# Kernel optimization log

Measured on AMD Instinct MI355X. Metric: run time of the kernel, lower is better.

Reference implementation:

```python
import jax, jax.numpy as jnp
import numpy as np

B, S, D, F, T, NS, L, H = 8, 1024, 1024, 4096, 64, 512, 32, 16
TAG_RATE = 0.5      # config.tagging_rate
GSR = 0.5           # config.gate_scaling_rate
ATT_EPS = 1e-12     # config.layer_norm_eps (att_norm)
ENC_EPS = 1e-5      # torch TransformerEncoderLayer default


def _ln(x, g, b, eps):
    m = x.mean(-1, keepdims=True)
    v = x.var(-1, keepdims=True)
    return (x - m) * jax.lax.rsqrt(v + eps) * g + b


def _rope(x):
    # standard rotary embedding over the full hidden dim
    d = x.shape[-1]
    s = x.shape[1]
    inv = 1.0 / (10000.0 ** (jnp.arange(0, d, 2, dtype=jnp.float32) / d))
    ang = jnp.arange(s, dtype=jnp.float32)[:, None] * inv[None, :]  # [S, D/2]
    sin, cos = jnp.sin(ang), jnp.cos(ang)
    x1, x2 = x[..., 0::2], x[..., 1::2]
    return jnp.stack([x1 * cos - x2 * sin, x1 * sin + x2 * cos], axis=-1).reshape(x.shape)


def setup_inputs() -> dict:
    key = jax.random.key(0)
    ks = jax.random.split(key, 24)
    p = lambda k, shp: (0.02 * jax.random.normal(k, shp, dtype=jnp.float32))
    inp = {
        'word_embedding': jax.random.normal(ks[0], (B, S, D), dtype=jnp.float32),
        'attention_mask': jnp.ones((B, S), dtype=jnp.int32),
        'span_batch': jax.random.randint(ks[1], (NS,), 0, B, dtype=jnp.int32),
        'span_start': jax.random.randint(ks[2], (NS,), 0, S - L, dtype=jnp.int32),
        'span_tag': jax.random.randint(ks[3], (NS,), 0, T, dtype=jnp.int32),
        'tag_emb': p(ks[4], (T, D)),
        'gate_w': p(ks[5], (D, 1)),
        'gate_b': jnp.zeros((1,), jnp.float32),
        'attn_ln_g': jnp.ones((D,), jnp.float32),
        'attn_ln_b': jnp.zeros((D,), jnp.float32),
        'in_proj_w': p(ks[6], (3 * D, D)),
        'in_proj_b': jnp.zeros((3 * D,), jnp.float32),
        'out_proj_w': p(ks[7], (D, D)),
        'out_proj_b': jnp.zeros((D,), jnp.float32),
        'enc_ln1_g': jnp.ones((D,), jnp.float32),
        'enc_ln1_b': jnp.zeros((D,), jnp.float32),
        'lin1_w': p(ks[8], (F, D)),
        'lin1_b': jnp.zeros((F,), jnp.float32),
        'lin2_w': p(ks[9], (D, F)),
        'lin2_b': jnp.zeros((D,), jnp.float32),
        'enc_ln2_g': jnp.ones((D,), jnp.float32),
        'enc_ln2_b': jnp.zeros((D,), jnp.float32),
    }
    return inp


def _mha(x, pad, in_proj_w, in_proj_b, out_proj_w, out_proj_b):
    b, s, d = x.shape
    hd = d // H
    qkv = x @ in_proj_w.T + in_proj_b                       # [B,S,3D]
    q, k, v = jnp.split(qkv, 3, axis=-1)
    rs = lambda t: t.reshape(b, s, H, hd).transpose(0, 2, 1, 3)  # [B,H,S,hd]
    q, k, v = rs(q), rs(k), rs(v)
    scores = jnp.einsum('bhqd,bhkd->bhqk', q, k) / jnp.sqrt(jnp.float32(hd))
    scores = jnp.where(pad[:, None, None, :], jnp.float32(-1e30), scores)
    attn = jax.nn.softmax(scores, axis=-1)
    o = jnp.einsum('bhqk,bhkd->bhqd', attn, v).transpose(0, 2, 1, 3).reshape(b, s, d)
    return o @ out_proj_w.T + out_proj_b


def reference(word_embedding, attention_mask, span_batch, span_start, span_tag,
              tag_emb, gate_w, gate_b, attn_ln_g, attn_ln_b,
              in_proj_w, in_proj_b, out_proj_w, out_proj_b,
              enc_ln1_g, enc_ln1_b, lin1_w, lin1_b, lin2_w, lin2_b,
              enc_ln2_g, enc_ln2_b):
    raw = word_embedding                        # dropout off (eval)
    we = _rope(word_embedding)
    # ragged gather -> gate -> scatter-add over fixed-length spans
    tok = span_start[:, None] + jnp.arange(L, dtype=jnp.int32)[None, :]  # [NS,L]
    X = we[span_batch[:, None], tok]            # [NS,L,D]
    gate = GSR * jax.nn.sigmoid(X @ gate_w + gate_b) + (1.0 - GSR) / 2.0  # [NS,L,1]
    res = gate * tag_emb[span_tag][:, None, :] * jnp.float32(L)          # [NS,L,D]
    taged = jnp.zeros_like(word_embedding).at[span_batch[:, None], tok].add(res)
    out_emb = raw + taged * TAG_RATE            # if_merge_by_add
    out_emb = _ln(out_emb, attn_ln_g, attn_ln_b, ATT_EPS)
    pad = attention_mask == 0
    # torch TransformerEncoderLayer (post-norm, relu)
    a = _mha(out_emb, pad, in_proj_w, in_proj_b, out_proj_w, out_proj_b)
    x = _ln(out_emb + a, enc_ln1_g, enc_ln1_b, ENC_EPS)
    ff = jax.nn.relu(x @ lin1_w.T + lin1_b) @ lin2_w.T + lin2_b
    enc = _ln(x + ff, enc_ln2_g, enc_ln2_b, ENC_EPS)
    return enc + out_emb
```

## Files before the change

### kernel.cpp

```cpp
#include <hip/hip_runtime.h>

#define DEV __device__ __forceinline__

typedef short bf16x8 __attribute__((ext_vector_type(8)));
typedef float f32x4 __attribute__((ext_vector_type(4)));
typedef unsigned short u16;
typedef unsigned int u32;

typedef __attribute__((address_space(3))) void lds_void;
typedef __attribute__((address_space(1))) void gbl_void;

DEV void async_copy16(void* lds_dst, const void* g_src) {
    __builtin_amdgcn_global_load_lds((gbl_void*)g_src, (lds_void*)lds_dst, 16, 0, 0);
}

DEV u16 f2bf(float x) {
    u32 u = __float_as_uint(x);
    return (u16)((u + 0x7fffu + ((u >> 16) & 1u)) >> 16);
}
DEV u16 f2bf_fast(float x) {
    return (u16)((__float_as_uint(x) + 0x8000u) >> 16);
}
DEV float bf2f(u16 v) { return __uint_as_float(((u32)v) << 16); }

__global__ __launch_bounds__(256) void f2bf_kernel(const float* __restrict__ src,
                                                   u16* __restrict__ dst, int n4) {
    const int i = blockIdx.x * 256 + threadIdx.x;
    if (i < n4) {
        const float4 v = ((const float4*)src)[i];
        ushort4 o;
        o.x = f2bf(v.x); o.y = f2bf(v.y); o.z = f2bf(v.z); o.w = f2bf(v.w);
        ((ushort4*)dst)[i] = o;
    }
}

__global__ __launch_bounds__(256) void span_kernel(
    const float* __restrict__ we, const int* __restrict__ sb,
    const int* __restrict__ ss, const int* __restrict__ stg,
    const float* __restrict__ tag_emb, const float* __restrict__ gate_w,
    const float* __restrict__ gate_b, float* __restrict__ out_pre) {
    __shared__ float red[4];
    const int n = blockIdx.x >> 5;
    const int l = blockIdx.x & 31;
    const int t = threadIdx.x;
    const int b = sb[n];
    const int s = ss[n] + l;
    const int tag = stg[n];
    const long base = ((long)b * 1024 + s) * 1024;
    float dot = 0.f;
#pragma unroll
    for (int pp = 0; pp < 2; ++pp) {
        const int p = t + pp * 256;
        const float e1 = we[base + 2 * p];
        const float e2 = we[base + 2 * p + 1];
        const float inv = exp2f((float)p * (-13.287712379549449f / 512.0f));
        const float ang = (float)s * inv;
        const float sa = __sinf(ang), ca = __cosf(ang);
        const float r1 = e1 * ca - e2 * sa;
        const float r2 = e1 * sa + e2 * ca;
        dot += r1 * gate_w[2 * p] + r2 * gate_w[2 * p + 1];
    }
#pragma unroll
    for (int off = 32; off > 0; off >>= 1) dot += __shfl_xor(dot, off, 64);
    if ((t & 63) == 0) red[t >> 6] = dot;
    __syncthreads();
    const float z = red[0] + red[1] + red[2] + red[3] + gate_b[0];
    const float gate = 0.25f + 0.5f / (1.f + __expf(-z));
    const float coef = gate * 16.f;
    const float* te = tag_emb + (long)tag * 1024;
#pragma unroll
    for (int c = 0; c < 4; ++c) {
        const int d = t + c * 256;
        atomicAdd(&out_pre[base + d], coef * te[d]);
    }
}

template <bool WRITE_F32, bool WRITE_BF, bool FINAL>
__global__ __launch_bounds__(256) void ln_kernel(
    const float* __restrict__ X, const float* __restrict__ g,
    const float* __restrict__ bta, float eps, float* __restrict__ Yf,
    u16* __restrict__ Ybf, const u16* __restrict__ addend) {
    __shared__ float red[8];
    const long row = blockIdx.x;
    const int t = threadIdx.x;
    const float4 x = ((const float4*)(X + row * 1024))[t];
    float s = x.x + x.y + x.z + x.w;
#pragma unroll
    for (int off = 32; off > 0; off >>= 1) s += __shfl_xor(s, off, 64);
    if ((t & 63) == 0) red[t >> 6] = s;
    __syncthreads();
    const float mean = (red[0] + red[1] + red[2] + red[3]) * (1.f / 1024.f);
    float4 dx;
    dx.x = x.x - mean; dx.y = x.y - mean; dx.z = x.z - mean; dx.w = x.w - mean;
    float ss = dx.x * dx.x + dx.y * dx.y + dx.z * dx.z + dx.w * dx.w;
#pragma unroll
    for (int off = 32; off > 0; off >>= 1) ss += __shfl_xor(ss, off, 64);
    if ((t & 63) == 0) red[4 + (t >> 6)] = ss;
    __syncthreads();
    const float var = (red[4] + red[5] + red[6] + red[7]) * (1.f / 1024.f);
    const float rstd = rsqrtf(var + eps);
    const float4 gv = ((const float4*)g)[t];
    const float4 bv = ((const float4*)bta)[t];
    float4 y;
    y.x = dx.x * rstd * gv.x + bv.x;
    y.y = dx.y * rstd * gv.y + bv.y;
    y.z = dx.z * rstd * gv.z + bv.z;
    y.w = dx.w * rstd * gv.w + bv.w;
    if (FINAL) {
        const ushort4 a = ((const ushort4*)(addend + row * 1024))[t];
        y.x += bf2f(a.x); y.y += bf2f(a.y); y.z += bf2f(a.z); y.w += bf2f(a.w);
    }
    if (WRITE_F32) ((float4*)(Yf + row * 1024))[t] = y;
    if (WRITE_BF) {
        ushort4 o;
        o.x = f2bf(y.x); o.y = f2bf(y.y); o.z = f2bf(y.z); o.w = f2bf(y.w);
        ((ushort4*)(Ybf + row * 1024))[t] = o;
    }
}

template <bool OUT_BF16, bool RELU, bool HAS_RES>
__global__ __launch_bounds__(256, 2) void gemm_nt(
    const u16* __restrict__ A, const u16* __restrict__ B,
    const float* __restrict__ bias, const u16* __restrict__ res,
    void* __restrict__ Cout, int N, int K) {
    __shared__ u16 Al[8192];
    __shared__ u16 Bl[8192];
    const int tid = threadIdx.x;
    const int wave = tid >> 6;
    const int lane = tid & 63;
    const int quad = lane >> 4;
    const int lq = lane & 15;
    const int wm = wave >> 1;
    const int wn = wave & 1;
    const long rowBase = (long)blockIdx.x * 128;
    const long colBase = (long)blockIdx.y * 128;

    f32x4 acc[4][4];
    const f32x4 fzero = {0.f, 0.f, 0.f, 0.f};
#pragma unroll
    for (int i = 0; i < 4; ++i)
#pragma unroll
        for (int j = 0; j < 4; ++j) acc[i][j] = fzero;

    const int rX = tid >> 3;
    const int pX = (tid & 7) ^ (rX & 7);
    const u16* gA = A + (rowBase + rX) * (long)K + pX * 8;
    const u16* gB = B + (colBase + rX) * (long)K + pX * 8;
    u16* ldsA = Al + wave * 512;
    u16* ldsB = Bl + wave * 512;

    for (int kt = 0; kt < K; kt += 64) {
        __syncthreads();
#pragma unroll
        for (int c = 0; c < 4; ++c) {
            async_copy16(ldsA + c * 2048, gA + (long)c * 32 * K + kt);
            async_copy16(ldsB + c * 2048, gB + (long)c * 32 * K + kt);
        }
        __syncthreads();
#pragma unroll
        for (int ks = 0; ks < 2; ++ks) {
            bf16x8 af[4], bfr[4];
#pragma unroll
            for (int i = 0; i < 4; ++i) {
                const int r = wm * 64 + i * 16 + lq;
                af[i] = *(const bf16x8*)&Al[r * 64 + (((ks * 4 + quad) ^ (lq & 7)) * 8)];
            }
#pragma unroll
            for (int j = 0; j < 4; ++j) {
                const int r = wn * 64 + j * 16 + lq;
                bfr[j] = *(const bf16x8*)&Bl[r * 64 + (((ks * 4 + quad) ^ (lq & 7)) * 8)];
            }
#pragma unroll
            for (int i = 0; i < 4; ++i)
#pragma unroll
                for (int j = 0; j < 4; ++j)
                    acc[i][j] = __builtin_amdgcn_mfma_f32_16x16x32_bf16(
                        af[i], bfr[j], acc[i][j], 0, 0, 0);
        }
    }

    float biasv[4];
#pragma unroll
    for (int j = 0; j < 4; ++j) biasv[j] = bias[colBase + wn * 64 + j * 16 + lq];
#pragma unroll
    for (int i = 0; i < 4; ++i) {
        const long grow = rowBase + wm * 64 + i * 16 + quad * 4;
#pragma unroll
        for (int j = 0; j < 4; ++j) {
            const long gcol = colBase + wn * 64 + j * 16 + lq;
#pragma unroll
            for (int r = 0; r < 4; ++r) {
                float v = acc[i][j][r] + biasv[j];
                if (RELU) v = fmaxf(v, 0.f);
                if (HAS_RES) v += bf2f(res[(grow + r) * N + gcol]);
                if (OUT_BF16)
                    ((u16*)Cout)[(grow + r) * N + gcol] = f2bf(v);
                else
                    ((float*)Cout)[(grow + r) * N + gcol] = v;
            }
        }
    }
}

template <bool OUT_BF16, bool RELU, bool HAS_RES>
__global__ __launch_bounds__(256, 4) void gemm_nt_m64(
    const u16* __restrict__ A, const u16* __restrict__ B,
    const float* __restrict__ bias, const u16* __restrict__ res,
    void* __restrict__ Cout, int N, int K) {
    __shared__ u16 Al[4096];
    __shared__ u16 Bl[8192];
    const int tid = threadIdx.x;
    const int wave = tid >> 6;
    const int lane = tid & 63;
    const int quad = lane >> 4;
    const int lq = lane & 15;
    const int wm = wave >> 1;
    const int wn = wave & 1;
    const long rowBase = (long)blockIdx.x * 64;
    const long colBase = (long)blockIdx.y * 128;

    f32x4 acc[2][4];
    const f32x4 fzero = {0.f, 0.f, 0.f, 0.f};
#pragma unroll
    for (int i = 0; i < 2; ++i)
#pragma unroll
        for (int j = 0; j < 4; ++j) acc[i][j] = fzero;

    const int rX = tid >> 3;
    const int pX = (tid & 7) ^ (rX & 7);
    const u16* gA = A + (rowBase + rX) * (long)K + pX * 8;
    const u16* gB = B + (colBase + rX) * (long)K + pX * 8;
    u16* ldsA = Al + wave * 512;
    u16* ldsB = Bl + wave * 512;

    for (int kt = 0; kt < K; kt += 64) {
        __syncthreads();
#pragma unroll
        for (int c = 0; c < 2; ++c)
            async_copy16(ldsA + c * 2048, gA + (long)c * 32 * K + kt);
#pragma unroll
        for (int c = 0; c < 4; ++c)
            async_copy16(ldsB + c * 2048, gB + (long)c * 32 * K + kt);
        __syncthreads();
#pragma unroll
        for (int ks = 0; ks < 2; ++ks) {
            bf16x8 af[2], bfr[4];
#pragma unroll
            for (int i = 0; i < 2; ++i) {
                const int r = wm * 32 + i * 16 + lq;
                af[i] = *(const bf16x8*)&Al[r * 64 + (((ks * 4 + quad) ^ (lq & 7)) * 8)];
            }
#pragma unroll
            for (int j = 0; j < 4; ++j) {
                const int r = wn * 64 + j * 16 + lq;
                bfr[j] = *(const bf16x8*)&Bl[r * 64 + (((ks * 4 + quad) ^ (lq & 7)) * 8)];
            }
#pragma unroll
            for (int i = 0; i < 2; ++i)
#pragma unroll
                for (int j = 0; j < 4; ++j)
                    acc[i][j] = __builtin_amdgcn_mfma_f32_16x16x32_bf16(
                        af[i], bfr[j], acc[i][j], 0, 0, 0);
        }
    }

    float biasv[4];
#pragma unroll
    for (int j = 0; j < 4; ++j) biasv[j] = bias[colBase + wn * 64 + j * 16 + lq];
#pragma unroll
    for (int i = 0; i < 2; ++i) {
        const long grow = rowBase + wm * 32 + i * 16 + quad * 4;
#pragma unroll
        for (int j = 0; j < 4; ++j) {
            const long gcol = colBase + wn * 64 + j * 16 + lq;
#pragma unroll
            for (int r = 0; r < 4; ++r) {
                float v = acc[i][j][r] + biasv[j];
                if (RELU) v = fmaxf(v, 0.f);
                if (HAS_RES) v += bf2f(res[(grow + r) * N + gcol]);
                if (OUT_BF16)
                    ((u16*)Cout)[(grow + r) * N + gcol] = f2bf(v);
                else
                    ((float*)Cout)[(grow + r) * N + gcol] = v;
            }
        }
    }
}

__global__ __launch_bounds__(256) void vtrans_kernel(const u16* __restrict__ QKV,
                                                     u16* __restrict__ Vt) {
    __shared__ u16 tile[64][72];
    const int bid = blockIdx.x;
    const int st = bid & 15;
    const int h = (bid >> 4) & 15;
    const int b = bid >> 8;
    const int t = threadIdx.x;
    const int sl = t >> 2;
    const int dc = (t & 3) * 16;
    const u16* src = QKV + ((long)(b * 1024 + st * 64 + sl)) * 3072 + 2048 + h * 64 + dc;
    *(uint4*)&tile[sl][dc] = *(const uint4*)src;
    *(uint4*)&tile[sl][dc + 8] = *(const uint4*)(src + 8);
    __syncthreads();
    const int dl = t >> 2;
    const int sc = (t & 3) * 16;
    union { u16 u[16]; uint4 q[2]; } tmp;
#pragma unroll
    for (int i = 0; i < 16; ++i) tmp.u[i] = tile[sc + i][dl];
    u16* dst = Vt + ((long)(b * 16 + h) * 64 + dl) * 1024 + st * 64 + sc;
    *(uint4*)dst = tmp.q[0];
    *(uint4*)(dst + 8) = tmp.q[1];
}

__global__ __launch_bounds__(256, 4) void attn_kernel(
    const u16* __restrict__ QKV, const u16* __restrict__ Vt,
    const int* __restrict__ mask, u16* __restrict__ Out) {
    __shared__ u16 KL[4096];
    __shared__ u16 VL[4096];
    __shared__ u16 PL[4][16 * 72];
    const int tid = threadIdx.x;
    const int wid = tid >> 6;
    const int lane = tid & 63;
    const int quad = lane >> 4;
    const int lq = lane & 15;
    const int slot0 = quad ^ (lq & 7);
    const int slot1 = slot0 ^ 4;

    const int bid = blockIdx.x;
    const int qb = bid & 7;
    const int h = (bid >> 3) & 15;
    const int b = bid >> 7;
    const int qbase = qb * 128 + wid * 32;

    bf16x8 aq[2][2];
#pragma unroll
    for (int t = 0; t < 2; ++t) {
        const u16* qp = QKV + ((long)(b * 1024 + qbase + t * 16 + lq)) * 3072 +
                        h * 64 + quad * 8;
        aq[t][0] = *(const bf16x8*)qp;
        aq[t][1] = *(const bf16x8*)(qp + 32);
    }

    const int c0 = tid, c1 = 256 + tid;
    const int r0 = c0 >> 3, j0 = (c0 & 7) ^ (r0 & 7);
    const int r1 = c1 >> 3, j1 = (c1 & 7) ^ (r1 & 7);
    const u16* srcK0 = QKV + ((long)(b * 1024 + r0)) * 3072 + 1024 + h * 64 + j0 * 8;
    const u16* srcK1 = QKV + ((long)(b * 1024 + r1)) * 3072 + 1024 + h * 64 + j1 * 8;
    const u16* srcV0 = Vt + ((long)(b * 16 + h) * 64 + r0) * 1024 + j0 * 8;
    const u16* srcV1 = Vt + ((long)(b * 16 + h) * 64 + r1) * 1024 + j1 * 8;
    u16* ldsK0 = KL + wid * 512;
    u16* ldsK1 = KL + 2048 + wid * 512;
    u16* ldsV0 = VL + wid * 512;
    u16* ldsV1 = VL + 2048 + wid * 512;

    const f32x4 fzero = {0.f, 0.f, 0.f, 0.f};
    f32x4 acc[2][4];
#pragma unroll
    for (int t = 0; t < 2; ++t)
#pragma unroll
        for (int j = 0; j < 4; ++j) acc[t][j] = fzero;
    float lsum[2][4] = {{0.f, 0.f, 0.f, 0.f}, {0.f, 0.f, 0.f, 0.f}};
    u16* myP = PL[wid];
    const int* mrow = mask + b * 1024;

    for (int kt = 0; kt < 1024; kt += 64) {
        __syncthreads();
        async_copy16(ldsK0, srcK0 + (long)kt * 3072);
        async_copy16(ldsK1, srcK1 + (long)kt * 3072);
        async_copy16(ldsV0, srcV0 + kt);
        async_copy16(ldsV1, srcV1 + kt);
        __syncthreads();

        bf16x8 kf0[4], kf1[4];
#pragma unroll
        for (int ct = 0; ct < 4; ++ct) {
            const int rowb = (ct * 16 + lq) * 64;
            kf0[ct] = *(const bf16x8*)&KL[rowb + slot0 * 8];
            kf1[ct] = *(const bf16x8*)&KL[rowb + slot1 * 8];
        }
        float mw[4];
#pragma unroll
        for (int ct = 0; ct < 4; ++ct) mw[ct] = mrow[kt + ct * 16 + lq] ? 1.f : 0.f;

#pragma unroll
        for (int t = 0; t < 2; ++t) {
            f32x4 s[4];
#pragma unroll
            for (int ct = 0; ct < 4; ++ct) {
                s[ct] = __builtin_amdgcn_mfma_f32_16x16x32_bf16(aq[t][0], kf0[ct],
                                                                fzero, 0, 0, 0);
                s[ct] = __builtin_amdgcn_mfma_f32_16x16x32_bf16(aq[t][1], kf1[ct],
                                                                s[ct], 0, 0, 0);
            }
            asm volatile("s_waitcnt lgkmcnt(0)" ::: "memory");
#pragma unroll
            for (int ct = 0; ct < 4; ++ct)
#pragma unroll
                for (int r = 0; r < 4; ++r) {
                    const float p = mw[ct] * __expf(s[ct][r] * 0.125f);
                    lsum[t][r] += p;
                    myP[(quad * 4 + r) * 72 + ct * 16 + lq] = f2bf_fast(p);
                }
            asm volatile("s_waitcnt lgkmcnt(0)" ::: "memory");
            const bf16x8 pf0 = *(const bf16x8*)&myP[lq * 72 + quad * 8];
            const bf16x8 pf1 = *(const bf16x8*)&myP[lq * 72 + 32 + quad * 8];
#pragma unroll
            for (int j = 0; j < 4; ++j) {
                const int rowb = (j * 16 + lq) * 64;
                const bf16x8 vf0 = *(const bf16x8*)&VL[rowb + slot0 * 8];
                const bf16x8 vf1 = *(const bf16x8*)&VL[rowb + slot1 * 8];
                acc[t][j] = __builtin_amdgcn_mfma_f32_16x16x32_bf16(pf0, vf0,
                                                                    acc[t][j], 0, 0, 0);
                acc[t][j] = __builtin_amdgcn_mfma_f32_16x16x32_bf16(pf1, vf1,
                                                                    acc[t][j], 0, 0, 0);
            }
        }
    }

#pragma unroll
    for (int t = 0; t < 2; ++t) {
        float inv[4];
#pragma unroll
        for (int r = 0; r < 4; ++r) {
            float l = lsum[t][r];
#pragma unroll
            for (int off = 1; off < 16; off <<= 1) l += __shfl_xor(l, off, 16);
            inv[r] = 1.f / l;
        }
        const long orow = (long)b * 1024 + qbase + t * 16 + quad * 4;
#pragma unroll
        for (int j = 0; j < 4; ++j)
#pragma unroll
            for (int r = 0; r < 4; ++r)
                Out[(orow + r) * 1024 + h * 64 + j * 16 + lq] =
                    f2bf_fast(acc[t][j][r] * inv[r]);
    }
}

extern "C" void kernel_launch(void* const* d_in, const int* in_sizes, int n_in,
                              void* d_out, int out_size, void* d_ws, size_t ws_size,
                              hipStream_t stream) {
    const float* we        = (const float*)d_in[0];
    const int*   amask     = (const int*)d_in[1];
    const int*   span_b    = (const int*)d_in[2];
    const int*   span_s    = (const int*)d_in[3];
    const int*   span_t    = (const int*)d_in[4];
    const float* tag_emb   = (const float*)d_in[5];
    const float* gate_w    = (const float*)d_in[6];
    const float* gate_b    = (const float*)d_in[7];
    const float* attn_ln_g = (const float*)d_in[8];
    const float* attn_ln_b = (const float*)d_in[9];
    const float* in_proj_w = (const float*)d_in[10];
    const float* in_proj_b = (const float*)d_in[11];
    const float* out_proj_w= (const float*)d_in[12];
    const float* out_proj_b= (const float*)d_in[13];
    const float* enc1_g    = (const float*)d_in[14];
    const float* enc1_b    = (const float*)d_in[15];
    const float* lin1_w    = (const float*)d_in[16];
    const float* lin1_b    = (const float*)d_in[17];
    const float* lin2_w    = (const float*)d_in[18];
    const float* lin2_b    = (const float*)d_in[19];
    const float* enc2_g    = (const float*)d_in[20];
    const float* enc2_b    = (const float*)d_in[21];
    float* out = (float*)d_out;

    char* ws = (char*)d_ws;
    size_t off = 0;
    auto alloc = [&](size_t bytes) {
        void* p = ws + off;
        off += (bytes + 255) & ~(size_t)255;
        return p;
    };
    const size_t MT = 8192;
    u16* oe_bf   = (u16*)alloc(MT * 1024 * 2);
    u16* ax_bf   = (u16*)alloc(MT * 1024 * 2);
    char* region = (char*)alloc((size_t)67108864);
    u16* qkv_bf  = (u16*)region;
    u16* vt_bf   = (u16*)(region + (size_t)MT * 3072 * 2);
    u16* ff1_bf  = (u16*)region;
    u16* wb_inproj  = (u16*)alloc((size_t)3072 * 1024 * 2);
    u16* wb_outproj = (u16*)alloc((size_t)1024 * 1024 * 2);
    u16* wb_lin1    = (u16*)alloc((size_t)4096 * 1024 * 2);
    u16* wb_lin2    = (u16*)alloc((size_t)1024 * 4096 * 2);

    hipMemcpyAsync(out, we, MT * 1024 * 4, hipMemcpyDeviceToDevice, stream);
    f2bf_kernel<<<3072, 256, 0, stream>>>(in_proj_w, wb_inproj, 3072 * 1024 / 4);
    f2bf_kernel<<<1024, 256, 0, stream>>>(out_proj_w, wb_outproj, 1024 * 1024 / 4);
    f2bf_kernel<<<4096, 256, 0, stream>>>(lin1_w, wb_lin1, 4096 * 1024 / 4);
    f2bf_kernel<<<4096, 256, 0, stream>>>(lin2_w, wb_lin2, 1024 * 4096 / 4);
    span_kernel<<<16384, 256, 0, stream>>>(we, span_b, span_s, span_t, tag_emb,
                                           gate_w, gate_b, out);
    ln_kernel<false, true, false><<<8192, 256, 0, stream>>>(
        out, attn_ln_g, attn_ln_b, 1e-12f, nullptr, oe_bf, nullptr);
    dim3 g1(64, 24);
    gemm_nt<true, false, false><<<g1, 256, 0, stream>>>(oe_bf, wb_inproj, in_proj_b,
                                                        nullptr, qkv_bf, 3072, 1024);
    vtrans_kernel<<<2048, 256, 0, stream>>>(qkv_bf, vt_bf);
    attn_kernel<<<1024, 256, 0, stream>>>(qkv_bf, vt_bf, amask, ax_bf);
    dim3 g2(128, 8);
    gemm_nt_m64<false, false, true><<<g2, 256, 0, stream>>>(
        ax_bf, wb_outproj, out_proj_b, oe_bf, out, 1024, 1024);
    ln_kernel<false, true, false><<<8192, 256, 0, stream>>>(
        out, enc1_g, enc1_b, 1e-5f, nullptr, ax_bf, nullptr);
    dim3 g3(64, 32);
    gemm_nt<true, true, false><<<g3, 256, 0, stream>>>(ax_bf, wb_lin1, lin1_b,
                                                       nullptr, ff1_bf, 4096, 1024);
    gemm_nt_m64<false, false, true><<<g2, 256, 0, stream>>>(
        ff1_bf, wb_lin2, lin2_b, ax_bf, out, 1024, 4096);
    ln_kernel<true, false, true><<<8192, 256, 0, stream>>>(
        out, enc2_g, enc2_b, 1e-5f, out, nullptr, oe_bf);
}
```

Measured before the change: 550.1 us.

## Use split-K 128x128 GEMM with atomic accumulation for N=1024 projections

```diff
diff --git a/kernel.cpp b/kernel.cpp
--- a/kernel.cpp
+++ b/kernel.cpp
@@ -32,6 +32,21 @@
         o.x = f2bf(v.x); o.y = f2bf(v.y); o.z = f2bf(v.z); o.w = f2bf(v.w);
         ((ushort4*)dst)[i] = o;
     }
+}
+
+__global__ __launch_bounds__(256) void bias_res_init(
+    const float* __restrict__ bias, const u16* __restrict__ res,
+    float* __restrict__ out) {
+    const int i = blockIdx.x * 256 + threadIdx.x;
+    const int col4 = i & 255;
+    const float4 b = ((const float4*)bias)[col4];
+    const ushort4 r = ((const ushort4*)res)[i];
+    float4 o;
+    o.x = b.x + bf2f(r.x);
+    o.y = b.y + bf2f(r.y);
+    o.z = b.z + bf2f(r.z);
+    o.w = b.w + bf2f(r.w);
+    ((float4*)out)[i] = o;
 }
 
 __global__ __launch_bounds__(256) void span_kernel(
@@ -202,12 +217,10 @@
     }
 }
 
-template <bool OUT_BF16, bool RELU, bool HAS_RES>
-__global__ __launch_bounds__(256, 4) void gemm_nt_m64(
+__global__ __launch_bounds__(256, 2) void gemm_nt_sk(
     const u16* __restrict__ A, const u16* __restrict__ B,
-    const float* __restrict__ bias, const u16* __restrict__ res,
-    void* __restrict__ Cout, int N, int K) {
-    __shared__ u16 Al[4096];
+    float* __restrict__ Cout, int N, int K) {
+    __shared__ u16 Al[8192];
     __shared__ u16 Bl[8192];
     const int tid = threadIdx.x;
     const int wave = tid >> 6;
@@ -216,13 +229,15 @@
     const int lq = lane & 15;
     const int wm = wave >> 1;
     const int wn = wave & 1;
-    const long rowBase = (long)blockIdx.x * 64;
+    const long rowBase = (long)blockIdx.x * 128;
     const long colBase = (long)blockIdx.y * 128;
-
-    f32x4 acc[2][4];
+    const int kHalf = K >> 1;
+    const int k0 = blockIdx.z * kHalf;
+
+    f32x4 acc[4][4];
     const f32x4 fzero = {0.f, 0.f, 0.f, 0.f};
 #pragma unroll
-    for (int i = 0; i < 2; ++i)
+    for (int i = 0; i < 4; ++i)
 #pragma unroll
         for (int j = 0; j < 4; ++j) acc[i][j] = fzero;
 
@@ -233,21 +248,20 @@
     u16* ldsA = Al + wave * 512;
     u16* ldsB = Bl + wave * 512;
 
-    for (int kt = 0; kt < K; kt += 64) {
+    for (int kt = k0; kt < k0 + kHalf; kt += 64) {
         __syncthreads();
 #pragma unroll
-        for (int c = 0; c < 2; ++c)
+        for (int c = 0; c < 4; ++c) {
             async_copy16(ldsA + c * 2048, gA + (long)c * 32 * K + kt);
-#pragma unroll
-        for (int c = 0; c < 4; ++c)
             async_copy16(ldsB + c * 2048, gB + (long)c * 32 * K + kt);
+        }
         __syncthreads();
 #pragma unroll
         for (int ks = 0; ks < 2; ++ks) {
-            bf16x8 af[2], bfr[4];
-#pragma unroll
-            for (int i = 0; i < 2; ++i) {
-                const int r = wm * 32 + i * 16 + lq;
+            bf16x8 af[4], bfr[4];
+#pragma unroll
+            for (int i = 0; i < 4; ++i) {
+                const int r = wm * 64 + i * 16 + lq;
                 af[i] = *(const bf16x8*)&Al[r * 64 + (((ks * 4 + quad) ^ (lq & 7)) * 8)];
             }
 #pragma unroll
@@ -256,7 +270,7 @@
                 bfr[j] = *(const bf16x8*)&Bl[r * 64 + (((ks * 4 + quad) ^ (lq & 7)) * 8)];
             }
 #pragma unroll
-            for (int i = 0; i < 2; ++i)
+            for (int i = 0; i < 4; ++i)
 #pragma unroll
                 for (int j = 0; j < 4; ++j)
                     acc[i][j] = __builtin_amdgcn_mfma_f32_16x16x32_bf16(
@@ -264,25 +278,15 @@
         }
     }
 
-    float biasv[4];
-#pragma unroll
-    for (int j = 0; j < 4; ++j) biasv[j] = bias[colBase + wn * 64 + j * 16 + lq];
-#pragma unroll
-    for (int i = 0; i < 2; ++i) {
-        const long grow = rowBase + wm * 32 + i * 16 + quad * 4;
+#pragma unroll
+    for (int i = 0; i < 4; ++i) {
+        const long grow = rowBase + wm * 64 + i * 16 + quad * 4;
 #pragma unroll
         for (int j = 0; j < 4; ++j) {
             const long gcol = colBase + wn * 64 + j * 16 + lq;
 #pragma unroll
-            for (int r = 0; r < 4; ++r) {
-                float v = acc[i][j][r] + biasv[j];
-                if (RELU) v = fmaxf(v, 0.f);
-                if (HAS_RES) v += bf2f(res[(grow + r) * N + gcol]);
-                if (OUT_BF16)
-                    ((u16*)Cout)[(grow + r) * N + gcol] = f2bf(v);
-                else
-                    ((float*)Cout)[(grow + r) * N + gcol] = v;
-            }
+            for (int r = 0; r < 4; ++r)
+                atomicAdd(&Cout[(grow + r) * N + gcol], acc[i][j][r]);
         }
     }
 }
@@ -496,16 +500,16 @@
                                                         nullptr, qkv_bf, 3072, 1024);
     vtrans_kernel<<<2048, 256, 0, stream>>>(qkv_bf, vt_bf);
     attn_kernel<<<1024, 256, 0, stream>>>(qkv_bf, vt_bf, amask, ax_bf);
-    dim3 g2(128, 8);
-    gemm_nt_m64<false, false, true><<<g2, 256, 0, stream>>>(
-        ax_bf, wb_outproj, out_proj_b, oe_bf, out, 1024, 1024);
+    bias_res_init<<<8192, 256, 0, stream>>>(out_proj_b, oe_bf, out);
+    dim3 g2(64, 8, 2);
+    gemm_nt_sk<<<g2, 256, 0, stream>>>(ax_bf, wb_outproj, out, 1024, 1024);
     ln_kernel<false, true, false><<<8192, 256, 0, stream>>>(
         out, enc1_g, enc1_b, 1e-5f, nullptr, ax_bf, nullptr);
     dim3 g3(64, 32);
     gemm_nt<true, true, false><<<g3, 256, 0, stream>>>(ax_bf, wb_lin1, lin1_b,
                                                        nullptr, ff1_bf, 4096, 1024);
-    gemm_nt_m64<false, false, true><<<g2, 256, 0, stream>>>(
-        ff1_bf, wb_lin2, lin2_b, ax_bf, out, 1024, 4096);
+    bias_res_init<<<8192, 256, 0, stream>>>(lin2_b, ax_bf, out);
+    gemm_nt_sk<<<g2, 256, 0, stream>>>(ff1_bf, wb_lin2, out, 1024, 4096);
     ln_kernel<true, false, true><<<8192, 256, 0, stream>>>(
         out, enc2_g, enc2_b, 1e-5f, out, nullptr, oe_bf);
 }
```

Result: slower. 641.1 us (+16.6%).
